# Kernel tuning notes

Measured on AMD Instinct MI355X. Metric: run time of the kernel, lower is better.

The kernel has to match this reference:

```python
import jax, jax.numpy as jnp
import numpy as np

IN, H = 512, 1024
EPS = 1e-5

def _ln(x, g, b):
    mu = jnp.mean(x, axis=-1, keepdims=True)
    var = jnp.mean(jnp.square(x - mu), axis=-1, keepdims=True)
    return (x - mu) * jax.lax.rsqrt(var + EPS) * g + b

def setup_inputs() -> dict:
    key = jax.random.key(0)
    ks = jax.random.split(key, 8)
    B = 8192
    x = jax.random.normal(ks[0], (B, IN), jnp.float32)
    h_prev = jax.random.normal(ks[1], (B, H), jnp.float32)
    c_prev = jax.random.normal(ks[2], (B, H), jnp.float32)
    # Xavier-uniform weights (torch Linear: weight [out, in])
    lim_i = float(np.sqrt(6.0 / (IN + 4 * H)))
    lim_h = float(np.sqrt(6.0 / (H + 4 * H)))
    Wi = jax.random.uniform(ks[3], (4 * H, IN), jnp.float32, -lim_i, lim_i)
    Wh = jax.random.uniform(ks[4], (4 * H, H), jnp.float32, -lim_h, lim_h)
    # biases zero-ish with forget-gate slice set to 1.0 (matches _initialize_weights)
    bi = jnp.zeros((4 * H,), jnp.float32).at[H:2 * H].set(1.0)
    bh = jnp.zeros((4 * H,), jnp.float32).at[H:2 * H].set(1.0)
    g_in = jnp.ones((4 * H,), jnp.float32); b_in = jnp.zeros((4 * H,), jnp.float32)
    g_hid = jnp.ones((4 * H,), jnp.float32); b_hid = jnp.zeros((4 * H,), jnp.float32)
    g_cell = jnp.ones((H,), jnp.float32); b_cell = jnp.zeros((H,), jnp.float32)
    return {"x": x, "h_prev": h_prev, "c_prev": c_prev,
            "Wi": Wi, "bi": bi, "Wh": Wh, "bh": bh,
            "g_in": g_in, "b_in": b_in, "g_hid": g_hid, "b_hid": b_hid,
            "g_cell": g_cell, "b_cell": b_cell}

def reference(x, h_prev, c_prev, Wi, bi, Wh, bh, g_in, b_in, g_hid, b_hid, g_cell, b_cell):
    input_proj = _ln(x @ Wi.T + bi, g_in, b_in)          # [B, 4H]
    hidden_proj = _ln(h_prev @ Wh.T + bh, g_hid, b_hid)  # [B, 4H]
    combined = input_proj + hidden_proj
    i, f, g, o = jnp.split(combined, 4, axis=1)
    i = jax.nn.sigmoid(i); f = jax.nn.sigmoid(f)
    g = jnp.tanh(g); o = jax.nn.sigmoid(o)
    c_new = f * c_prev + i * g
    h_new = o * jnp.tanh(_ln(c_new, g_cell, b_cell))
    return (h_new, c_new)
```

## Files before the change

### kernel.cpp

```cpp
#include <hip/hip_runtime.h>
#include <hip/hip_bf16.h>

#define EPS 1e-5f

typedef __attribute__((ext_vector_type(8))) short short8;
typedef __attribute__((ext_vector_type(4))) short short4v;
typedef __attribute__((ext_vector_type(4))) float floatx4;

__device__ inline float b2f(short s) {
    union { unsigned u; float f; } v;
    v.u = ((unsigned)(unsigned short)s) << 16;
    return v.f;
}
__device__ inline float sigmoidf_(float x) { return 1.f / (1.f + __expf(-x)); }
__device__ inline float tanhf_(float x) { return 1.f - 2.f / (__expf(2.f * x) + 1.f); }

__device__ inline void load_lds16(const void* g, void* l) {
    __builtin_amdgcn_global_load_lds(
        (const __attribute__((address_space(1))) void*)g,
        (__attribute__((address_space(3))) void*)l, 16, 0, 0);
}

__global__ __launch_bounds__(256)
void cvt_bf16(const float* __restrict__ s0, __hip_bfloat16* __restrict__ d0, int n0_,
              const float* __restrict__ s1, __hip_bfloat16* __restrict__ d1, int n1_,
              const float* __restrict__ s2, __hip_bfloat16* __restrict__ d2, int n2_,
              const float* __restrict__ s3, __hip_bfloat16* __restrict__ d3, int n3_) {
    const float* s; __hip_bfloat16* d; int n;
    switch (blockIdx.y) {
        case 0:  s = s0; d = d0; n = n0_; break;
        case 1:  s = s1; d = d1; n = n1_; break;
        case 2:  s = s2; d = d2; n = n2_; break;
        default: s = s3; d = d3; n = n3_; break;
    }
    const int idx = (blockIdx.x * 256 + threadIdx.x) * 8;
    if (idx < n) {
        float4 v0 = *(const float4*)(s + idx);
        float4 v1 = *(const float4*)(s + idx + 4);
        union { short8 sv; __hip_bfloat16 h[8]; } u;
        u.h[0] = __float2bfloat16(v0.x); u.h[1] = __float2bfloat16(v0.y);
        u.h[2] = __float2bfloat16(v0.z); u.h[3] = __float2bfloat16(v0.w);
        u.h[4] = __float2bfloat16(v1.x); u.h[5] = __float2bfloat16(v1.y);
        u.h[6] = __float2bfloat16(v1.z); u.h[7] = __float2bfloat16(v1.w);
        *(short8*)(d + idx) = u.sv;
    }
}

__global__ __launch_bounds__(256, 3)
void gemm_dual(const __hip_bfloat16* __restrict__ A0, const __hip_bfloat16* __restrict__ W0,
               const float* __restrict__ bias0, __hip_bfloat16* __restrict__ out0, int K0,
               const __hip_bfloat16* __restrict__ A1, const __hip_bfloat16* __restrict__ W1,
               const float* __restrict__ bias1, __hip_bfloat16* __restrict__ out1, int K1) {
    __shared__ alignas(16) __hip_bfloat16 smem[17408];
    __hip_bfloat16* sA = smem;
    __hip_bfloat16* sB = smem + 8192;

    const __hip_bfloat16* A;  const __hip_bfloat16* W;
    const float* bias;        __hip_bfloat16* out;  int K;
    if (blockIdx.z == 0) { A = A0; W = W0; bias = bias0; out = out0; K = K0; }
    else                 { A = A1; W = W1; bias = bias1; out = out1; K = K1; }

    const int t    = threadIdx.x;
    const int lane = t & 63;
    const int wave = t >> 6;
    const int quad = lane >> 4;
    const int rl   = lane & 15;
    const int wm   = (wave >> 1) * 64;
    const int wn   = (wave & 1) * 64;
    const int m0   = blockIdx.y * 128;
    const int n0   = blockIdx.x * 128;

    floatx4 acc[4][4];
    #pragma unroll
    for (int i = 0; i < 4; ++i)
        #pragma unroll
        for (int j = 0; j < 4; ++j)
            acc[i][j] = (floatx4){0.f, 0.f, 0.f, 0.f};

    int srow[4], scol[4];
    #pragma unroll
    for (int i = 0; i < 4; ++i) {
        const int cl  = (wave * 4 + i) * 64 + lane;
        const int row = cl >> 3;
        srow[i] = row;
        scol[i] = ((cl & 7) ^ (row & 7)) * 8;
    }

    for (int k0 = 0; k0 < K; k0 += 64) {
        __syncthreads();
        #pragma unroll
        for (int i = 0; i < 4; ++i) {
            load_lds16(A + (size_t)(m0 + srow[i]) * K + k0 + scol[i], sA + (wave * 4 + i) * 512);
            load_lds16(W + (size_t)(n0 + srow[i]) * K + k0 + scol[i], sB + (wave * 4 + i) * 512);
        }
        __syncthreads();
        #pragma unroll
        for (int kk = 0; kk < 2; ++kk) {
            short8 aF[4], bF[4];
            #pragma unroll
            for (int i = 0; i < 4; ++i) {
                const int r = wm + i * 16 + rl;
                const int c = kk * 4 + quad;
                aF[i] = *(const short8*)(sA + (r * 8 + (c ^ (r & 7))) * 8);
            }
            #pragma unroll
            for (int j = 0; j < 4; ++j) {
                const int r = wn + j * 16 + rl;
                const int c = kk * 4 + quad;
                bF[j] = *(const short8*)(sB + (r * 8 + (c ^ (r & 7))) * 8);
            }
            #pragma unroll
            for (int i = 0; i < 4; ++i)
                #pragma unroll
                for (int j = 0; j < 4; ++j)
                    acc[i][j] = __builtin_amdgcn_mfma_f32_16x16x32_bf16(aF[i], bF[j], acc[i][j], 0, 0, 0);
        }
    }

    __syncthreads();
    #pragma unroll
    for (int j = 0; j < 4; ++j) {
        const int col = wn + j * 16 + rl;
        const float bv = bias[n0 + col];
        #pragma unroll
        for (int i = 0; i < 4; ++i) {
            const int rbase = wm + i * 16 + quad * 4;
            #pragma unroll
            for (int r = 0; r < 4; ++r)
                smem[(rbase + r) * 136 + col] = __float2bfloat16(acc[i][j][r] + bv);
        }
    }
    __syncthreads();
    #pragma unroll
    for (int p = 0; p < 8; ++p) {
        const int ch  = p * 256 + t;
        const int row = ch >> 4;
        const int c8  = (ch & 15) * 8;
        short8 v = *(const short8*)(smem + row * 136 + c8);
        *(short8*)(out + (size_t)(m0 + row) * 4096 + n0 + c8) = v;
    }
}

__global__ __launch_bounds__(256)
void ln_gates(const __hip_bfloat16* __restrict__ Pi, const __hip_bfloat16* __restrict__ Ph,
              const float* __restrict__ c_prev,
              const float* __restrict__ g_in, const float* __restrict__ b_in,
              const float* __restrict__ g_hid, const float* __restrict__ b_hid,
              const float* __restrict__ g_cell, const float* __restrict__ b_cell,
              float* __restrict__ h_out, float* __restrict__ c_out) {
    const int t    = threadIdx.x;
    const int half = t >> 7;
    const int tt   = t & 127;
    const int wave = t >> 6;
    const int row  = blockIdx.x * 2 + half;
    __shared__ float sred[4][6];

    const __hip_bfloat16* pi = Pi + (size_t)row * 4096;
    const __hip_bfloat16* ph = Ph + (size_t)row * 4096;
    const int j0 = tt * 8;

    float fpi[4][8], fph[4][8];
    float si = 0.f, sqi = 0.f, sh = 0.f, sqh = 0.f;
    #pragma unroll
    for (int g = 0; g < 4; ++g) {
        short8 vi = *(const short8*)(pi + g * 1024 + j0);
        short8 vh = *(const short8*)(ph + g * 1024 + j0);
        #pragma unroll
        for (int e = 0; e < 8; ++e) {
            const float a = b2f(vi[e]); fpi[g][e] = a; si += a; sqi += a * a;
            const float b = b2f(vh[e]); fph[g][e] = b; sh += b; sqh += b * b;
        }
    }
    floatx4 cp0 = *(const floatx4*)(c_prev + (size_t)row * 1024 + j0);
    floatx4 cp1 = *(const floatx4*)(c_prev + (size_t)row * 1024 + j0 + 4);

    #pragma unroll
    for (int mask = 1; mask <= 32; mask <<= 1) {
        si += __shfl_xor(si, mask); sqi += __shfl_xor(sqi, mask);
        sh += __shfl_xor(sh, mask); sqh += __shfl_xor(sqh, mask);
    }
    if ((t & 63) == 0) {
        sred[wave][0] = si; sred[wave][1] = sqi;
        sred[wave][2] = sh; sred[wave][3] = sqh;
    }
    __syncthreads();
    const int wb = half * 2;
    si  = sred[wb][0] + sred[wb + 1][0];
    sqi = sred[wb][1] + sred[wb + 1][1];
    sh  = sred[wb][2] + sred[wb + 1][2];
    sqh = sred[wb][3] + sred[wb + 1][3];

    const float mu_i = si * (1.f / 4096.f);
    const float rs_i = rsqrtf(sqi * (1.f / 4096.f) - mu_i * mu_i + EPS);
    const float mu_h = sh * (1.f / 4096.f);
    const float rs_h = rsqrtf(sqh * (1.f / 4096.f) - mu_h * mu_h + EPS);

    float comb[4][8];
    #pragma unroll
    for (int g = 0; g < 4; ++g) {
        const int col = g * 1024 + j0;
        floatx4 gi0  = *(const floatx4*)(g_in  + col);
        floatx4 gi1  = *(const floatx4*)(g_in  + col + 4);
        floatx4 bi0  = *(const floatx4*)(b_in  + col);
        floatx4 bi1  = *(const floatx4*)(b_in  + col + 4);
        floatx4 gh0  = *(const floatx4*)(g_hid + col);
        floatx4 gh1  = *(const floatx4*)(g_hid + col + 4);
        floatx4 bh0  = *(const floatx4*)(b_hid + col);
        floatx4 bh1  = *(const floatx4*)(b_hid + col + 4);
        #pragma unroll
        for (int e = 0; e < 4; ++e) {
            comb[g][e]     = (fpi[g][e]     - mu_i) * rs_i * gi0[e] + bi0[e]
                           + (fph[g][e]     - mu_h) * rs_h * gh0[e] + bh0[e];
            comb[g][e + 4] = (fpi[g][e + 4] - mu_i) * rs_i * gi1[e] + bi1[e]
                           + (fph[g][e + 4] - mu_h) * rs_h * gh1[e] + bh1[e];
        }
    }

    float cn[8], ov[8];
    float sc = 0.f, scq = 0.f;
    #pragma unroll
    for (int e = 0; e < 8; ++e) {
        const float iv = sigmoidf_(comb[0][e]);
        const float fv = sigmoidf_(comb[1][e]);
        const float gv = tanhf_(comb[2][e]);
        ov[e] = sigmoidf_(comb[3][e]);
        const float cpv = (e < 4) ? cp0[e] : cp1[e - 4];
        const float c = fv * cpv + iv * gv;
        cn[e] = c; sc += c; scq += c * c;
    }
    #pragma unroll
    for (int mask = 1; mask <= 32; mask <<= 1) {
        sc += __shfl_xor(sc, mask); scq += __shfl_xor(scq, mask);
    }
    if ((t & 63) == 0) { sred[wave][4] = sc; sred[wave][5] = scq; }
    __syncthreads();
    sc  = sred[wb][4] + sred[wb + 1][4];
    scq = sred[wb][5] + sred[wb + 1][5];
    const float mu_c = sc * (1.f / 1024.f);
    const float rs_c = rsqrtf(scq * (1.f / 1024.f) - mu_c * mu_c + EPS);

    floatx4 gc0 = *(const floatx4*)(g_cell + j0);
    floatx4 gc1 = *(const floatx4*)(g_cell + j0 + 4);
    floatx4 bc0 = *(const floatx4*)(b_cell + j0);
    floatx4 bc1 = *(const floatx4*)(b_cell + j0 + 4);
    floatx4 hv0, hv1, cv0, cv1;
    #pragma unroll
    for (int e = 0; e < 4; ++e) {
        const float nc0 = (cn[e]     - mu_c) * rs_c * gc0[e] + bc0[e];
        const float nc1 = (cn[e + 4] - mu_c) * rs_c * gc1[e] + bc1[e];
        hv0[e] = ov[e] * tanhf_(nc0);
        hv1[e] = ov[e + 4] * tanhf_(nc1);
        cv0[e] = cn[e];
        cv1[e] = cn[e + 4];
    }
    float* hp = h_out + (size_t)row * 1024 + j0;
    float* cpout = c_out + (size_t)row * 1024 + j0;
    *(floatx4*)(hp) = hv0;     *(floatx4*)(hp + 4) = hv1;
    *(floatx4*)(cpout) = cv0;  *(floatx4*)(cpout + 4) = cv1;
}

extern "C" void kernel_launch(void* const* d_in, const int* in_sizes, int n_in,
                              void* d_out, int out_size, void* d_ws, size_t ws_size,
                              hipStream_t stream) {
    const float* x      = (const float*)d_in[0];
    const float* h_prev = (const float*)d_in[1];
    const float* c_prev = (const float*)d_in[2];
    const float* Wi     = (const float*)d_in[3];
    const float* bi     = (const float*)d_in[4];
    const float* Wh     = (const float*)d_in[5];
    const float* bh     = (const float*)d_in[6];
    const float* g_in   = (const float*)d_in[7];
    const float* b_in   = (const float*)d_in[8];
    const float* g_hid  = (const float*)d_in[9];
    const float* b_hid  = (const float*)d_in[10];
    const float* g_cell = (const float*)d_in[11];
    const float* b_cell = (const float*)d_in[12];

    __hip_bfloat16* Pi = (__hip_bfloat16*)d_ws;
    __hip_bfloat16* Ph = Pi + (size_t)8192 * 4096;

    const int NX = 8192 * 512, NH = 8192 * 1024, NWI = 4096 * 512, NWH = 4096 * 1024;
    __hip_bfloat16* xb  = (__hip_bfloat16*)d_out;
    __hip_bfloat16* hb  = xb + NX;
    __hip_bfloat16* Wib = hb + NH;
    __hip_bfloat16* Whb = Wib + NWI;

    float* h_out = (float*)d_out;
    float* c_out = h_out + (size_t)8192 * 1024;

    hipLaunchKernelGGL(cvt_bf16, dim3(4096, 4), dim3(256), 0, stream,
                       x, xb, NX, h_prev, hb, NH, Wi, Wib, NWI, Wh, Whb, NWH);

    hipLaunchKernelGGL(gemm_dual, dim3(32, 64, 2), dim3(256), 0, stream,
                       xb, Wib, bi, Pi, 512,
                       hb, Whb, bh, Ph, 1024);

    hipLaunchKernelGGL(ln_gates, dim3(4096), dim3(256), 0, stream, Pi, Ph, c_prev,
                       g_in, b_in, g_hid, b_hid, g_cell, b_cell, h_out, c_out);
}
```

Baseline: 319.6 us.

## Rewrite dual GEMM with 256x256 tiles, double-buffered LDS and ping-pong phases

After: 342.9 us. 1.07x slower.

```diff
diff --git a/kernel.cpp b/kernel.cpp
--- a/kernel.cpp
+++ b/kernel.cpp
@@ -4,7 +4,6 @@
 #define EPS 1e-5f
 
 typedef __attribute__((ext_vector_type(8))) short short8;
-typedef __attribute__((ext_vector_type(4))) short short4v;
 typedef __attribute__((ext_vector_type(4))) float floatx4;
 
 __device__ inline float b2f(short s) {
@@ -46,18 +45,61 @@
     }
 }
 
-__global__ __launch_bounds__(256, 3)
+#define STAGE_HALF(P, BASE, H, KZ, DSTB) do {                                   \
+    const int rs0_ = (H) * 128 + r0;                                            \
+    load_lds16((P) + (size_t)((BASE) + rs0_) * K + (KZ) + ((c0 ^ (rs0_ & 7)) << 3), \
+               smem + (DSTB) + ((((H) << 10) + (wave << 6)) << 3));             \
+    const int rs1_ = (H) * 128 + 64 + r0;                                       \
+    load_lds16((P) + (size_t)((BASE) + rs1_) * K + (KZ) + ((c0 ^ (rs1_ & 7)) << 3), \
+               smem + (DSTB) + ((((H) << 10) + 512 + (wave << 6)) << 3));       \
+} while (0)
+
+#define PHASE_Q(QQ, CURB, LASTP) do {                                           \
+    const int hm_ = ((QQ) >= 2) ? 1 : 0;                                        \
+    const int hn_ = ((QQ) == 1 || (QQ) == 2) ? 1 : 0;                           \
+    const __hip_bfloat16* At_ = smem + (CURB) * 32768;                          \
+    const __hip_bfloat16* Bt_ = smem + (CURB) * 32768 + 16384;                  \
+    short8 aF[2][4], bF[2][2];                                                  \
+    _Pragma("unroll")                                                           \
+    for (int kk = 0; kk < 2; ++kk) {                                            \
+        const int c_ = kk * 4 + quad;                                           \
+        _Pragma("unroll")                                                       \
+        for (int i = 0; i < 4; ++i) {                                           \
+            const int r_ = wm + hm_ * 64 + i * 16 + rl;                         \
+            aF[kk][i] = *(const short8*)(At_ + ((r_ * 8 + (c_ ^ (r_ & 7))) << 3)); \
+        }                                                                       \
+        _Pragma("unroll")                                                       \
+        for (int j = 0; j < 2; ++j) {                                           \
+            const int r_ = wn + hn_ * 32 + j * 16 + rl;                         \
+            bF[kk][j] = *(const short8*)(Bt_ + ((r_ * 8 + (c_ ^ (r_ & 7))) << 3)); \
+        }                                                                       \
+    }                                                                           \
+    __builtin_amdgcn_s_barrier();                                               \
+    asm volatile("s_waitcnt lgkmcnt(0)" ::: "memory");                          \
+    __builtin_amdgcn_s_setprio(1);                                              \
+    _Pragma("unroll")                                                           \
+    for (int kk = 0; kk < 2; ++kk)                                              \
+        _Pragma("unroll")                                                       \
+        for (int i = 0; i < 4; ++i)                                             \
+            _Pragma("unroll")                                                   \
+            for (int j = 0; j < 2; ++j)                                         \
+                acc[hm_ * 4 + i][hn_ * 2 + j] = __builtin_amdgcn_mfma_f32_16x16x32_bf16( \
+                    aF[kk][i], bF[kk][j], acc[hm_ * 4 + i][hn_ * 2 + j], 0, 0, 0); \
+    __builtin_amdgcn_s_setprio(0);                                              \
+    if (LASTP) asm volatile("s_waitcnt vmcnt(0)" ::: "memory");                 \
+    __builtin_amdgcn_s_barrier();                                               \
+} while (0)
+
+__global__ __launch_bounds__(512, 2)
 void gemm_dual(const __hip_bfloat16* __restrict__ A0, const __hip_bfloat16* __restrict__ W0,
                const float* __restrict__ bias0, __hip_bfloat16* __restrict__ out0, int K0,
                const __hip_bfloat16* __restrict__ A1, const __hip_bfloat16* __restrict__ W1,
                const float* __restrict__ bias1, __hip_bfloat16* __restrict__ out1, int K1) {
-    __shared__ alignas(16) __hip_bfloat16 smem[17408];
-    __hip_bfloat16* sA = smem;
-    __hip_bfloat16* sB = smem + 8192;
+    __shared__ alignas(16) __hip_bfloat16 smem[65536];
 
     const __hip_bfloat16* A;  const __hip_bfloat16* W;
     const float* bias;        __hip_bfloat16* out;  int K;
-    if (blockIdx.z == 0) { A = A0; W = W0; bias = bias0; out = out0; K = K0; }
+    if (blockIdx.y == 0) { A = A0; W = W0; bias = bias0; out = out0; K = K0; }
     else                 { A = A1; W = W1; bias = bias1; out = out1; K = K1; }
 
     const int t    = threadIdx.x;
@@ -65,79 +107,77 @@
     const int wave = t >> 6;
     const int quad = lane >> 4;
     const int rl   = lane & 15;
-    const int wm   = (wave >> 1) * 64;
-    const int wn   = (wave & 1) * 64;
-    const int m0   = blockIdx.y * 128;
-    const int n0   = blockIdx.x * 128;
-
-    floatx4 acc[4][4];
-    #pragma unroll
-    for (int i = 0; i < 4; ++i)
+    const int wm   = (wave >> 2) * 128;
+    const int wn   = (wave & 3) * 64;
+
+    const int id  = blockIdx.x;
+    const int swz = (id & 7) * 64 + (id >> 3);
+    const int m0  = (swz >> 4) * 256;
+    const int n0  = (swz & 15) * 256;
+
+    const int r0 = t >> 3;
+    const int c0 = t & 7;
+
+    floatx4 acc[8][4];
+    #pragma unroll
+    for (int i = 0; i < 8; ++i)
         #pragma unroll
         for (int j = 0; j < 4; ++j)
             acc[i][j] = (floatx4){0.f, 0.f, 0.f, 0.f};
 
-    int srow[4], scol[4];
-    #pragma unroll
-    for (int i = 0; i < 4; ++i) {
-        const int cl  = (wave * 4 + i) * 64 + lane;
-        const int row = cl >> 3;
-        srow[i] = row;
-        scol[i] = ((cl & 7) ^ (row & 7)) * 8;
-    }
-
-    for (int k0 = 0; k0 < K; k0 += 64) {
+    STAGE_HALF(A, m0, 0, 0, 0);
+    STAGE_HALF(W, n0, 0, 0, 16384);
+    STAGE_HALF(W, n0, 1, 0, 16384);
+    STAGE_HALF(A, m0, 1, 0, 0);
+    asm volatile("s_waitcnt vmcnt(0)" ::: "memory");
+    __builtin_amdgcn_s_barrier();
+
+    const int NT = K >> 6;
+    for (int T = 0; T < NT; ++T) {
+        const int cur = T & 1;
+        if (T + 1 < NT) {
+            const int kn = (T + 1) << 6;
+            const int ab = (cur ^ 1) * 32768;
+            const int bb = ab + 16384;
+            STAGE_HALF(A, m0, 0, kn, ab);
+            STAGE_HALF(W, n0, 0, kn, bb);
+            STAGE_HALF(W, n0, 1, kn, bb);
+            STAGE_HALF(A, m0, 1, kn, ab);
+        }
+        PHASE_Q(0, cur, 0);
+        PHASE_Q(1, cur, 0);
+        PHASE_Q(2, cur, 0);
+        PHASE_Q(3, cur, 1);
+    }
+
+    __syncthreads();
+    const int wh = wave >> 2;
+    #pragma unroll
+    for (int h = 0; h < 2; ++h) {
+        if (wh == h) {
+            #pragma unroll
+            for (int jc = 0; jc < 4; ++jc) {
+                const int col = wn + jc * 16 + rl;
+                const float bv = bias[n0 + col];
+                #pragma unroll
+                for (int im = 0; im < 8; ++im) {
+                    const int rloc = im * 16 + quad * 4;
+                    #pragma unroll
+                    for (int rr = 0; rr < 4; ++rr)
+                        smem[(rloc + rr) * 264 + col] = __float2bfloat16(acc[im][jc][rr] + bv);
+                }
+            }
+        }
         __syncthreads();
         #pragma unroll
-        for (int i = 0; i < 4; ++i) {
-            load_lds16(A + (size_t)(m0 + srow[i]) * K + k0 + scol[i], sA + (wave * 4 + i) * 512);
-            load_lds16(W + (size_t)(n0 + srow[i]) * K + k0 + scol[i], sB + (wave * 4 + i) * 512);
+        for (int p = 0; p < 8; ++p) {
+            const int ch  = p * 512 + t;
+            const int row = ch >> 5;
+            const int c8  = (ch & 31) << 3;
+            short8 v = *(const short8*)(smem + row * 264 + c8);
+            *(short8*)(out + (size_t)(m0 + h * 128 + row) * 4096 + n0 + c8) = v;
         }
         __syncthreads();
-        #pragma unroll
-        for (int kk = 0; kk < 2; ++kk) {
-            short8 aF[4], bF[4];
-            #pragma unroll
-            for (int i = 0; i < 4; ++i) {
-                const int r = wm + i * 16 + rl;
-                const int c = kk * 4 + quad;
-                aF[i] = *(const short8*)(sA + (r * 8 + (c ^ (r & 7))) * 8);
-            }
-            #pragma unroll
-            for (int j = 0; j < 4; ++j) {
-                const int r = wn + j * 16 + rl;
-                const int c = kk * 4 + quad;
-                bF[j] = *(const short8*)(sB + (r * 8 + (c ^ (r & 7))) * 8);
-            }
-            #pragma unroll
-            for (int i = 0; i < 4; ++i)
-                #pragma unroll
-                for (int j = 0; j < 4; ++j)
-                    acc[i][j] = __builtin_amdgcn_mfma_f32_16x16x32_bf16(aF[i], bF[j], acc[i][j], 0, 0, 0);
-        }
-    }
-
-    __syncthreads();
-    #pragma unroll
-    for (int j = 0; j < 4; ++j) {
-        const int col = wn + j * 16 + rl;
-        const float bv = bias[n0 + col];
-        #pragma unroll
-        for (int i = 0; i < 4; ++i) {
-            const int rbase = wm + i * 16 + quad * 4;
-            #pragma unroll
-            for (int r = 0; r < 4; ++r)
-                smem[(rbase + r) * 136 + col] = __float2bfloat16(acc[i][j][r] + bv);
-        }
-    }
-    __syncthreads();
-    #pragma unroll
-    for (int p = 0; p < 8; ++p) {
-        const int ch  = p * 256 + t;
-        const int row = ch >> 4;
-        const int c8  = (ch & 15) * 8;
-        short8 v = *(const short8*)(smem + row * 136 + c8);
-        *(short8*)(out + (size_t)(m0 + row) * 4096 + n0 + c8) = v;
     }
 }
 
@@ -291,7 +331,7 @@
     hipLaunchKernelGGL(cvt_bf16, dim3(4096, 4), dim3(256), 0, stream,
                        x, xb, NX, h_prev, hb, NH, Wi, Wib, NWI, Wh, Whb, NWH);
 
-    hipLaunchKernelGGL(gemm_dual, dim3(32, 64, 2), dim3(256), 0, stream,
+    hipLaunchKernelGGL(gemm_dual, dim3(512, 2), dim3(512), 0, stream,
                        xb, Wib, bi, Pi, 512,
                        hb, Whb, bh, Ph, 1024);
 
```
